# Kernel tuning notes

Hardware: AMD Instinct MI355X
Metric: run time of the kernel (lower is better)

Reference implementation:

```python
import jax, jax.numpy as jnp
import numpy as np

B, L, F, H, VOCAB = 32, 700, 4, 600, 2000  # batch, n_records(max_len), feats/record, hidden, vocab


def setup_inputs() -> dict:
    key = jax.random.key(0)
    ks = jax.random.split(key, 16)
    s = 0.02
    inp = {
        'records': jax.random.randint(ks[0], (B, L, F), 0, VOCAB, dtype=jnp.int64 if jax.config.jax_enable_x64 else jnp.int32),
        'index': jax.random.randint(ks[1], (B,), 0, L, dtype=jnp.int32),
        'emb': jax.random.normal(ks[2], (VOCAB, H), jnp.float32) * s,
        'W_relu': jax.random.normal(ks[3], (4 * H, H), jnp.float32) * s,
        'b_relu': jnp.zeros((H,), jnp.float32),
        'W_lin': jax.random.normal(ks[4], (H, H), jnp.float32) * s,
        'b_lin': jnp.zeros((H,), jnp.float32),
        'W_sig': jax.random.normal(ks[5], (2 * H, H), jnp.float32) * s,
        'b_sig': jnp.zeros((H,), jnp.float32),
        'W_ih': jax.random.normal(ks[6], (H, 4 * H), jnp.float32) * s,
        'W_hh': jax.random.normal(ks[7], (H, 4 * H), jnp.float32) * s,
        'b_ih': jnp.zeros((4 * H,), jnp.float32),
        'b_hh': jnp.zeros((4 * H,), jnp.float32),
        'W_log': jax.random.normal(ks[8], (H, L), jnp.float32) * s,
        'b_log': jnp.zeros((L,), jnp.float32),
    }
    return inp


def _select_content(records, emb, W_relu, b_relu, W_lin, b_lin, W_sig, b_sig):
    # embedding + concat of the 4 record features -> [B, L, 4H]
    embedded = emb[records]                               # [B, L, 4, H]
    emb_cat = embedded.reshape(records.shape[0], records.shape[1], -1)
    emb_relu = jax.nn.relu(emb_cat @ W_relu + b_relu)      # [B, L, H]
    emb_lin = emb_relu @ W_lin + b_lin                     # [B, L, H]
    pre_attn = jnp.einsum('bld,bmd->blm', emb_lin, emb_relu)  # [B, L, L]
    pad = (records.max(axis=2) == 0)                       # [B, L]
    mask = jnp.eye(records.shape[1], dtype=bool)[None] | pad[:, :, None] | pad[:, None, :]
    pre_attn = jnp.where(mask, -jnp.inf, pre_attn)
    attention = jax.nn.softmax(pre_attn, axis=2)
    emb_att = jnp.einsum('blm,bmd->bld', attention, emb_relu)  # [B, L, H]
    gate = jax.nn.sigmoid(jnp.concatenate([emb_relu, emb_att], axis=2) @ W_sig + b_sig)
    return gate * emb_relu                                 # selected_content [B, L, H]


def reference(records, index, emb, W_relu, b_relu, W_lin, b_lin, W_sig, b_sig,
              W_ih, W_hh, b_ih, b_hh, W_log, b_log):
    sc = _select_content(records, emb, W_relu, b_relu, W_lin, b_lin, W_sig, b_sig)
    # init_hidden
    hidden = jnp.mean(sc, axis=1)                          # [B, H]
    cell = jnp.zeros_like(hidden)
    pad_mask = (records.max(axis=2) == 0)                  # [B, L]
    # forward (one pointer step)
    b_idx = jnp.arange(records.shape[0])
    mask = pad_mask.at[b_idx, index].set(True)             # scatter_(1, index, 1)
    x = sc[b_idx, index]                                   # gather -> [B, H]
    gates = x @ W_ih + hidden @ W_hh + b_ih + b_hh         # [B, 4H]
    i, f, g, o = jnp.split(gates, 4, axis=1)               # torch LSTM gate order
    cell = jax.nn.sigmoid(f) * cell + jax.nn.sigmoid(i) * jnp.tanh(g)
    hidden = jax.nn.sigmoid(o) * jnp.tanh(cell)
    logits = hidden @ W_log + b_log                        # [B, max_len]
    masked = jnp.where(mask, -jnp.inf, logits)
    attention = jax.nn.log_softmax(masked, axis=1)         # [B, max_len]
    return attention, hidden, cell
```

## Files before the change

kernel.cpp:

```cpp
#include <hip/hip_runtime.h>
#include <math.h>

typedef unsigned short u16;
typedef _Float16 half8 __attribute__((ext_vector_type(8)));
typedef float f32x4 __attribute__((ext_vector_type(4)));

#define BB 32
#define LL 700
#define HH 600
#define VV 2000
#define H4 2400

#define O_SCAT   0L
#define O_LINH   57344000L
#define O_R1     86016000L
#define O_ATTNH  112896000L
#define O_ERT    144435200L
#define O_EMBH   171468800L
#define O_W2T    174028800L
#define O_WLT    177100800L
#define O_WST    177920000L
#define O_BL     179456000L
#define O_PAD    179458560L
#define O_GATES  179624960L
#define O_WIHT   179932160L
#define O_WLOGT  186076160L
#define O_XCAT   186977280L
#define O_HID16  187059200L
#define O_GLOG   187100160L

__device__ inline u16 f2h(float x) { _Float16 h = (_Float16)x; u16 u; __builtin_memcpy(&u, &h, 2); return u; }
__device__ inline float h2f(u16 u) { _Float16 h; __builtin_memcpy(&h, &u, 2); return (float)h; }
__device__ inline float to_f(float x) { return x; }
__device__ inline float to_f(u16 x) { return h2f(x); }

#define LROW 68
#define BUFSZ (128 * LROW)

template<int EPI>
__global__ __launch_bounds__(512, 4) void hgemm_k(
    const u16* __restrict__ A, const u16* __restrict__ B,
    float* __restrict__ C32, u16* __restrict__ C16,
    const float* __restrict__ bias, const u16* __restrict__ gate, int ldg,
    int M, int N, int Kp, int lda, int ldb, int ldc,
    long sA, long sB, long sC)
{
    const int bz = blockIdx.z;
    A += sA * bz;  B += sB * bz;
    if (EPI == 0) C32 += sC * bz; else C16 += sC * bz;

    __shared__ __align__(16) u16 As[2 * BUFSZ];
    __shared__ __align__(16) u16 Bs[2 * BUFSZ];

    const int tid  = threadIdx.x;

    const int nx = gridDim.x, ny = gridDim.y;
    const int bid = blockIdx.y * nx + blockIdx.x;
    const int fg  = ny >> 3;
    const int gsz = nx << 3;
    int m_i, n_i;
    if (bid < fg * gsz) {
        int g = bid / gsz, r = bid - g * gsz;
        m_i = (g << 3) + (r & 7);
        n_i = r >> 3;
    } else {
        m_i = bid / nx;
        n_i = bid - m_i * nx;
    }
    const int m0 = m_i << 7, n0 = n_i << 7;

    const int wave = tid >> 6, lane = tid & 63;
    const int wm = (wave >> 2) << 6;
    const int wn = (wave & 3) << 5;
    const int fr = lane & 15, q8 = (lane >> 4) << 3;

    const int lrow8 = lane >> 3;
    const int lcol8 = (lane & 7) << 3;
    int ar0 = m0 + (wave << 4) + lrow8;      if (ar0 > M - 1) ar0 = M - 1;
    int ar1 = m0 + (wave << 4) + 8 + lrow8;  if (ar1 > M - 1) ar1 = M - 1;
    int br0 = n0 + (wave << 4) + lrow8;      if (br0 > N - 1) br0 = N - 1;
    int br1 = n0 + (wave << 4) + 8 + lrow8;  if (br1 > N - 1) br1 = N - 1;
    const u16* gA0 = A + (long)ar0 * lda + lcol8;
    const u16* gA1 = A + (long)ar1 * lda + lcol8;
    const u16* gB0 = B + (long)br0 * ldb + lcol8;
    const u16* gB1 = B + (long)br1 * ldb + lcol8;
    const int lo0 = ((wave << 4) + lrow8) * LROW + lcol8;
    const int lo1 = lo0 + 8 * LROW;

    f32x4 acc[4][2];
    #pragma unroll
    for (int i = 0; i < 4; ++i)
        #pragma unroll
        for (int j = 0; j < 2; ++j) acc[i][j] = (f32x4)0.f;

    const int nk = Kp >> 6;
    uint4 pA0, pA1, pB0, pB1, qA0, qA1, qB0, qB1;

    pA0 = *(const uint4*)gA0;  pA1 = *(const uint4*)gA1;
    pB0 = *(const uint4*)gB0;  pB1 = *(const uint4*)gB1;
    *(uint4*)&As[lo0] = pA0;  *(uint4*)&As[lo1] = pA1;
    *(uint4*)&Bs[lo0] = pB0;  *(uint4*)&Bs[lo1] = pB1;
    if (nk > 1) {
        pA0 = *(const uint4*)(gA0 + 64);  pA1 = *(const uint4*)(gA1 + 64);
        pB0 = *(const uint4*)(gB0 + 64);  pB1 = *(const uint4*)(gB1 + 64);
    }
    __syncthreads();

    for (int s = 0; s < nk; ++s) {
        const int cur = (s & 1) * BUFSZ;
        if (s + 2 < nk) {
            const long ko = (long)(s + 2) << 6;
            qA0 = *(const uint4*)(gA0 + ko);  qA1 = *(const uint4*)(gA1 + ko);
            qB0 = *(const uint4*)(gB0 + ko);  qB1 = *(const uint4*)(gB1 + ko);
        }
        #pragma unroll
        for (int half = 0; half < 2; ++half) {
            const int kof = q8 + (half << 5);
            half8 af[4], bf[2];
            #pragma unroll
            for (int i = 0; i < 4; ++i) af[i] = *(const half8*)&As[cur + (wm + (i << 4) + fr) * LROW + kof];
            #pragma unroll
            for (int j = 0; j < 2; ++j) bf[j] = *(const half8*)&Bs[cur + (wn + (j << 4) + fr) * LROW + kof];
            #pragma unroll
            for (int i = 0; i < 4; ++i)
                #pragma unroll
                for (int j = 0; j < 2; ++j)
                    acc[i][j] = __builtin_amdgcn_mfma_f32_16x16x32_f16(af[i], bf[j], acc[i][j], 0, 0, 0);
        }
        if (s + 1 < nk) {
            const int nxt = ((s + 1) & 1) * BUFSZ;
            *(uint4*)&As[nxt + lo0] = pA0;  *(uint4*)&As[nxt + lo1] = pA1;
            *(uint4*)&Bs[nxt + lo0] = pB0;  *(uint4*)&Bs[nxt + lo1] = pB1;
        }
        pA0 = qA0;  pA1 = qA1;  pB0 = qB0;  pB1 = qB1;
        __syncthreads();
    }

    const int lr = (lane >> 4) << 2;
    #pragma unroll
    for (int j = 0; j < 2; ++j) {
        int n = n0 + wn + (j << 4) + fr;
        if (n >= N) continue;
        float bv = bias ? bias[n] : 0.f;
        #pragma unroll
        for (int i = 0; i < 4; ++i) {
            #pragma unroll
            for (int r = 0; r < 4; ++r) {
                int m = m0 + wm + (i << 4) + lr + r;
                if (m >= M) continue;
                long off = (long)m * ldc + n;
                float v = acc[i][j][r] + bv;
                if (EPI == 0) C32[off] = v;
                if (EPI == 1) C16[off] = f2h(v);
                if (EPI == 2) {
                    float sg = 1.f / (1.f + expf(-v));
                    C16[off] = f2h(sg * h2f(gate[(long)m * ldg + n]));
                }
            }
        }
    }
}

__global__ __launch_bounds__(256) void sgemm_k(
    const u16* __restrict__ A, const u16* __restrict__ B, float* __restrict__ C,
    int N, int Kseg, int lda, int ldb, int ldc)
{
    const int wave = threadIdx.x >> 6, lane = threadIdx.x & 63;
    const int fr = lane & 15, q8 = (lane >> 4) << 3;
    int n = blockIdx.x * 64 + wave * 16 + fr;
    int nc = (n < N) ? n : N - 1;
    const int k0 = blockIdx.y * Kseg;
    const u16* pa0 = A + (long)fr * lda + q8;
    const u16* pa1 = A + (long)(fr + 16) * lda + q8;
    const u16* pb  = B + (long)nc * ldb + q8;
    f32x4 acc0 = (f32x4)0.f, acc1 = (f32x4)0.f;
    #pragma unroll 2
    for (int k = k0; k < k0 + Kseg; k += 32) {
        half8 a0 = *(const half8*)(pa0 + k);
        half8 a1 = *(const half8*)(pa1 + k);
        half8 bv = *(const half8*)(pb + k);
        acc0 = __builtin_amdgcn_mfma_f32_16x16x32_f16(a0, bv, acc0, 0, 0, 0);
        acc1 = __builtin_amdgcn_mfma_f32_16x16x32_f16(a1, bv, acc1, 0, 0, 0);
    }
    if (n >= N) return;
    const int mr = (lane >> 4) << 2;
    #pragma unroll
    for (int r = 0; r < 4; ++r) {
        atomicAdd(&C[(long)(mr + r) * ldc + n], acc0[r]);
        atomicAdd(&C[(long)(mr + r + 16) * ldc + n], acc1[r]);
    }
}

__global__ __launch_bounds__(256) void prep_k(
    const float* __restrict__ emb, const float* __restrict__ W_relu,
    const float* __restrict__ W_lin, const float* __restrict__ W_sig,
    const float* __restrict__ W_ih, const float* __restrict__ W_hh,
    const float* __restrict__ W_log, const float* __restrict__ b_lin,
    const float* __restrict__ b_ih, const float* __restrict__ b_hh,
    const float* __restrict__ b_log,
    u16* __restrict__ embh, u16* __restrict__ w2t, u16* __restrict__ wlt,
    u16* __restrict__ wst, u16* __restrict__ wiht, u16* __restrict__ wlogt,
    float* __restrict__ bl640, float* __restrict__ gates, float* __restrict__ glog)
{
    __shared__ float t[32][33];
    const int z = blockIdx.z, bx = blockIdx.x, by = blockIdx.y;
    const int tid = threadIdx.x;

    if (z == 10) {
        int r = by * 32 + (tid >> 5), c = bx * 32 + (tid & 31);
        #pragma unroll
        for (int dy = 0; dy < 32; dy += 8) {
            int rr = r + dy;
            if (rr < VV && c < 640)
                embh[(long)rr * 640 + c] = (c < 600) ? f2h(emb[(long)rr * 600 + c]) : 0;
        }
        return;
    }
    if (z == 11) {
        long idx = ((long)bx * 75 + by) * 256 + tid;
        if (idx < 640) {
            bl640[idx] = (idx < 600) ? b_lin[idx] : 0.f;
        } else if (idx < 640 + (long)BB * H4) {
            long i = idx - 640;
            int n = (int)(i % H4);
            gates[i] = b_ih[n] + b_hh[n];
        } else if (idx < 640 + (long)BB * H4 + (long)BB * 704) {
            long i = idx - 640 - (long)BB * H4;
            int l = (int)(i % 704);
            glog[i] = (l < 700) ? b_log[l] : 0.f;
        }
        return;
    }

    const float* s; u16* d;
    int R, C, lds_, ldo, Rpad, Cpad;
    if (z < 4)      { s = W_relu + 360000L * z; d = w2t + 384000L * z;
                      R = 600; C = 600; lds_ = 600; ldo = 640;  Rpad = 640; Cpad = 600; }
    else if (z == 4){ s = W_lin;           d = wlt;
                      R = 600; C = 600; lds_ = 600; ldo = 640;  Rpad = 640; Cpad = 640; }
    else if (z == 5){ s = W_sig;           d = wst;
                      R = 600; C = 600; lds_ = 600; ldo = 1280; Rpad = 640; Cpad = 600; }
    else if (z == 6){ s = W_sig + 360000;  d = wst + 640;
                      R = 600; C = 600; lds_ = 600; ldo = 1280; Rpad = 640; Cpad = 600; }
    else if (z == 7){ s = W_ih;            d = wiht;
                      R = 600; C = H4;  lds_ = H4;  ldo = 1280; Rpad = 640; Cpad = H4; }
    else if (z == 8){ s = W_hh;            d = wiht + 640;
                      R = 600; C = H4;  lds_ = H4;  ldo = 1280; Rpad = 640; Cpad = H4; }
    else            { s = W_log;           d = wlogt;
                      R = 600; C = 700; lds_ = 700; ldo = 640;  Rpad = 640; Cpad = 704; }

    int r0 = bx * 32, c0 = by * 32;
    if (r0 >= Rpad || c0 >= Cpad) return;
    int tx = tid & 31, ty = tid >> 5;
    #pragma unroll
    for (int dy = 0; dy < 32; dy += 8) {
        int r = r0 + ty + dy, c = c0 + tx;
        t[ty + dy][tx] = (r < R && c < C) ? s[(long)r * lds_ + c] : 0.f;
    }
    __syncthreads();
    #pragma unroll
    for (int dy = 0; dy < 32; dy += 8) {
        int c = c0 + ty + dy, r = r0 + tx;
        if (r < Rpad && c < Cpad) d[(long)c * ldo + r] = f2h(t[tx][ty + dy]);
    }
}

template<typename T>
__global__ __launch_bounds__(256) void transpz_k(
    const T* __restrict__ s, u16* __restrict__ d,
    int R, int C, int lds_, int ldo, int Rpad, int Cpad, long zs_s, long zs_d)
{
    __shared__ float t[32][33];
    s += zs_s * blockIdx.z;  d += zs_d * blockIdx.z;
    int r0 = blockIdx.x * 32, c0 = blockIdx.y * 32;
    int tx = threadIdx.x & 31, ty = threadIdx.x >> 5;
    #pragma unroll
    for (int dy = 0; dy < 32; dy += 8) {
        int r = r0 + ty + dy, c = c0 + tx;
        t[ty + dy][tx] = (r < R && c < C) ? to_f(s[(long)r * lds_ + c]) : 0.f;
    }
    __syncthreads();
    #pragma unroll
    for (int dy = 0; dy < 32; dy += 8) {
        int c = c0 + ty + dy, r = r0 + tx;
        if (r < Rpad && c < Cpad) d[(long)c * ldo + r] = f2h(t[tx][ty + dy]);
    }
}

__global__ __launch_bounds__(320) void gather_relu_k(
    const int* __restrict__ rec, const u16* __restrict__ Ph,
    const float* __restrict__ b_relu, u16* __restrict__ scat, float* __restrict__ pad)
{
    int row = blockIdx.x;
    int t = threadIdx.x;
    int r0 = rec[row * 4 + 0], r1 = rec[row * 4 + 1];
    int r2 = rec[row * 4 + 2], r3 = rec[row * 4 + 3];
    u16* srow = scat + (long)row * 1280;
    if (t < 300) {
        int h = t << 1;
        uint a0 = *(const uint*)&Ph[(long)r0 * H4 + h];
        uint a1 = *(const uint*)&Ph[(long)r1 * H4 + 600 + h];
        uint a2 = *(const uint*)&Ph[(long)r2 * H4 + 1200 + h];
        uint a3 = *(const uint*)&Ph[(long)r3 * H4 + 1800 + h];
        float lo = b_relu[h]     + h2f((u16)a0) + h2f((u16)a1) + h2f((u16)a2) + h2f((u16)a3);
        float hi = b_relu[h + 1] + h2f((u16)(a0 >> 16)) + h2f((u16)(a1 >> 16))
                                 + h2f((u16)(a2 >> 16)) + h2f((u16)(a3 >> 16));
        uint o = (uint)f2h(fmaxf(lo, 0.f)) | ((uint)f2h(fmaxf(hi, 0.f)) << 16);
        *(uint*)&srow[h] = o;
    } else {
        int i = t - 300;
        *(uint*)&srow[600 + (i << 1)]  = 0;
        *(uint*)&srow[1240 + (i << 1)] = 0;
    }
    if (t == 0) {
        int mx = max(max(r0, r1), max(r2, r3));
        pad[row] = (mx == 0) ? 1.f : 0.f;
    }
}

__global__ __launch_bounds__(256) void softmax_w(u16* __restrict__ attnh,
                                                 const float* __restrict__ pad)
{
    const int wave = threadIdx.x >> 6, lane = threadIdx.x & 63;
    const int l = blockIdx.x * 4 + wave, b = blockIdx.y;
    u16* row = attnh + (long)b * (LL * 704) + (long)l * 704;
    const float* pb = pad + b * LL;
    const bool rowpad = pb[l] != 0.f;

    float v[12];
    float mx = -INFINITY;
    #pragma unroll
    for (int i = 0; i < 6; ++i) {
        int e0 = (lane + (i << 6)) << 1;
        float x0 = -INFINITY, x1 = -INFINITY;
        if (e0 < 704) {
            uint u = *(const uint*)&row[e0];
            if (e0 < LL && !(rowpad || e0 == l || pb[e0] != 0.f)) x0 = h2f((u16)u);
            int e1 = e0 + 1;
            if (e1 < LL && !(rowpad || e1 == l || pb[e1] != 0.f)) x1 = h2f((u16)(u >> 16));
        }
        v[2 * i] = x0;  v[2 * i + 1] = x1;
        mx = fmaxf(mx, fmaxf(x0, x1));
    }
    #pragma unroll
    for (int m = 32; m > 0; m >>= 1) mx = fmaxf(mx, __shfl_xor(mx, m));
    mx = fmaxf(mx, -1e30f);

    float sum = 0.f;
    #pragma unroll
    for (int i = 0; i < 12; ++i) { v[i] = expf(v[i] - mx); sum += v[i]; }
    #pragma unroll
    for (int m = 32; m > 0; m >>= 1) sum += __shfl_xor(sum, m);
    float inv = (sum > 0.f) ? 1.f / sum : 0.f;

    #pragma unroll
    for (int i = 0; i < 6; ++i) {
        int e0 = (lane + (i << 6)) << 1;
        if (e0 < 704) {
            uint u = (uint)f2h(v[2 * i] * inv) | ((uint)f2h(v[2 * i + 1] * inv) << 16);
            *(uint*)&row[e0] = u;
        }
    }
}

__global__ __launch_bounds__(256) void xcat_k(const u16* __restrict__ sc,
                                              const int* __restrict__ index,
                                              u16* __restrict__ xcat)
{
    int b = blockIdx.y;
    if (blockIdx.x == 3) {
        const u16* src = sc + ((long)b * LL + index[b]) * HH;
        u16* dst = xcat + b * 1280;
        for (int j = threadIdx.x; j < 1280; j += 256) {
            if (j < 600) dst[j] = src[j];
            else if (j < 640) dst[j] = 0;
            else if (j >= 1240) dst[j] = 0;
        }
        return;
    }
    int h = blockIdx.x * 256 + threadIdx.x;
    if (h >= HH) return;
    float s = 0.f;
    const u16* base = sc + (long)b * LL * HH + h;
    for (int l = 0; l < LL; ++l) s += h2f(base[(long)l * HH]);
    xcat[b * 1280 + 640 + h] = f2h(s * (1.f / 700.f));
}

__global__ void lstm_act_k(const float* __restrict__ gates,
                           float* __restrict__ out_hid, float* __restrict__ out_cell,
                           u16* __restrict__ hid16)
{
    int h = blockIdx.x * 256 + threadIdx.x;
    int b = blockIdx.y;
    if (h >= 640) return;
    if (h >= HH) { hid16[b * 640 + h] = 0; return; }
    const float* g = gates + b * H4;
    float gi = g[h], gg = g[1200 + h], go = g[1800 + h];
    float c = (1.f / (1.f + expf(-gi))) * tanhf(gg);
    float hd = (1.f / (1.f + expf(-go))) * tanhf(c);
    out_hid[b * HH + h] = hd;
    out_cell[b * HH + h] = c;
    hid16[b * 640 + h] = f2h(hd);
}

__global__ __launch_bounds__(256) void logsoftmax_k(const float* __restrict__ glog,
                                                    const float* __restrict__ pad,
                                                    const int* __restrict__ index,
                                                    float* __restrict__ out)
{
    int b = blockIdx.x;
    int t = threadIdx.x;
    int idx = index[b];
    __shared__ float red[256];
    float v[3];
    float mx = -INFINITY;
    #pragma unroll
    for (int ii = 0; ii < 3; ++ii) {
        int l = ii * 256 + t;
        float x = -INFINITY;
        if (l < LL && !(pad[b * LL + l] != 0.f || l == idx)) x = glog[b * 704 + l];
        v[ii] = x;
        mx = fmaxf(mx, x);
    }
    red[t] = mx; __syncthreads();
    for (int s = 128; s > 0; s >>= 1) {
        if (t < s) red[t] = fmaxf(red[t], red[t + s]);
        __syncthreads();
    }
    mx = red[0]; __syncthreads();
    float sum = 0.f;
    #pragma unroll
    for (int ii = 0; ii < 3; ++ii) {
        int l = ii * 256 + t;
        if (l < LL) sum += expf(v[ii] - mx);
    }
    red[t] = sum; __syncthreads();
    for (int s = 128; s > 0; s >>= 1) {
        if (t < s) red[t] += red[t + s];
        __syncthreads();
    }
    float lse = mx + logf(red[0]);
    #pragma unroll
    for (int ii = 0; ii < 3; ++ii) {
        int l = ii * 256 + t;
        if (l < LL) out[b * LL + l] = fmaxf(v[ii] - lse, -1e30f);
    }
}

extern "C" void kernel_launch(void* const* d_in, const int* in_sizes, int n_in,
                              void* d_out, int out_size, void* d_ws, size_t ws_size,
                              hipStream_t stream)
{
    const int*   records = (const int*)d_in[0];
    const int*   index   = (const int*)d_in[1];
    const float* emb     = (const float*)d_in[2];
    const float* W_relu  = (const float*)d_in[3];
    const float* b_relu  = (const float*)d_in[4];
    const float* W_lin   = (const float*)d_in[5];
    const float* b_lin   = (const float*)d_in[6];
    const float* W_sig   = (const float*)d_in[7];
    const float* b_sig   = (const float*)d_in[8];
    const float* W_ih    = (const float*)d_in[9];
    const float* W_hh    = (const float*)d_in[10];
    const float* b_ih    = (const float*)d_in[11];
    const float* b_hh    = (const float*)d_in[12];
    const float* W_log   = (const float*)d_in[13];
    const float* b_log   = (const float*)d_in[14];

    char* ws = (char*)d_ws;
    u16*   scat   = (u16*)(ws + O_SCAT);
    u16*   linh   = (u16*)(ws + O_LINH);
    u16*   Ph     = (u16*)(ws + O_R1);
    u16*   sc16   = (u16*)(ws + O_R1);
    u16*   attnh  = (u16*)(ws + O_ATTNH);
    u16*   erT    = (u16*)(ws + O_ERT);
    u16*   embh   = (u16*)(ws + O_EMBH);
    u16*   w2t    = (u16*)(ws + O_W2T);
    u16*   wlt    = (u16*)(ws + O_WLT);
    u16*   wst    = (u16*)(ws + O_WST);
    float* bl640  = (float*)(ws + O_BL);
    float* pad    = (float*)(ws + O_PAD);
    float* gates  = (float*)(ws + O_GATES);
    u16*   wiht   = (u16*)(ws + O_WIHT);
    u16*   wlogt  = (u16*)(ws + O_WLOGT);
    u16*   xcat   = (u16*)(ws + O_XCAT);
    u16*   hid16  = (u16*)(ws + O_HID16);
    float* glog   = (float*)(ws + O_GLOG);

    float* out      = (float*)d_out;
    float* out_attn = out;
    float* out_hid  = out + BB * LL;
    float* out_cell = out + BB * LL + BB * HH;

    prep_k<<<dim3(20, 75, 12), 256, 0, stream>>>(
        emb, W_relu, W_lin, W_sig, W_ih, W_hh, W_log, b_lin, b_ih, b_hh, b_log,
        embh, w2t, wlt, wst, wiht, wlogt, bl640, gates, glog);

    hgemm_k<1><<<dim3(19, 16, 1), 512, 0, stream>>>(
        embh, w2t, nullptr, Ph, nullptr, nullptr, 0,
        VV, H4, 640, 640, 640, H4, 0L, 0L, 0L);

    gather_relu_k<<<dim3(BB * LL), 320, 0, stream>>>(records, Ph, b_relu, scat, pad);

    hgemm_k<1><<<dim3(5, 175, 1), 512, 0, stream>>>(
        scat, wlt, nullptr, linh, bl640, nullptr, 0,
        BB * LL, 640, 640, 1280, 640, 640, 0L, 0L, 0L);

    hgemm_k<1><<<dim3(6, 6, BB), 512, 0, stream>>>(
        linh, scat, nullptr, attnh, nullptr, nullptr, 0,
        LL, LL, 640, 640, 1280, 704, (long)LL * 640, (long)LL * 1280, (long)LL * 704);

    softmax_w<<<dim3(175, BB), 256, 0, stream>>>(attnh, pad);

    transpz_k<u16><<<dim3(22, 19, BB), 256, 0, stream>>>(
        scat, erT, 700, 600, 1280, 704, 704, 600, (long)700 * 1280, (long)600 * 704);

    hgemm_k<1><<<dim3(5, 6, BB), 512, 0, stream>>>(
        attnh, erT, nullptr, scat + 640, nullptr, nullptr, 0,
        LL, HH, 704, 704, 704, 1280, (long)LL * 704, (long)HH * 704, (long)LL * 1280);

    hgemm_k<2><<<dim3(5, 175, 1), 512, 0, stream>>>(
        scat, wst, nullptr, sc16, b_sig, scat, 1280,
        BB * LL, HH, 1280, 1280, 1280, HH, 0L, 0L, 0L);

    xcat_k<<<dim3(4, BB), 256, 0, stream>>>(sc16, index, xcat);
    sgemm_k<<<dim3(38, 5), 256, 0, stream>>>(
        xcat, wiht, gates, H4, 256, 1280, 1280, H4);
    lstm_act_k<<<dim3(3, BB), 256, 0, stream>>>(gates, out_hid, out_cell, hid16);
    sgemm_k<<<dim3(11, 5), 256, 0, stream>>>(
        hid16, wlogt, glog, LL, 128, 640, 640, 704);
    logsoftmax_k<<<dim3(BB), 256, 0, stream>>>(glog, pad, index, out_attn);
}
```

Measured before the change: 454.4 us.

## Add 256x256-tile HGEMM with direct global-to-LDS loads for the main GEMMs

Adds a new fp16 MFMA GEMM kernel with 256x256 output tiles and 8 waves, each wave computing 128x64. It loads A and B straight into LDS with global_load_lds and interleaves those loads with the MFMA phases under explicit waitcnt and barrier control. Tiles are visited in grouped order for L2 reuse, and the work runs at raised wave priority. It replaces the older 128-tile kernel for the linear, attention-score, attention-apply and sigmoid-gate GEMMs, aiming for more data reuse per tile and better overlap of loads with compute. In exchange, the larger tiles waste more work on ragged edges (700 and 600 are not multiples of 256), give smaller grids, and depend on hand-written synchronisation being correct.

```diff
diff --git a/kernel.cpp b/kernel.cpp
--- a/kernel.cpp
+++ b/kernel.cpp
@@ -33,6 +33,149 @@
 __device__ inline float h2f(u16 u) { _Float16 h; __builtin_memcpy(&h, &u, 2); return (float)h; }
 __device__ inline float to_f(float x) { return x; }
 __device__ inline float to_f(u16 x) { return h2f(x); }
+
+__device__ __forceinline__ void gll16(const u16* g, u16* l) {
+    __builtin_amdgcn_global_load_lds(
+        (__attribute__((address_space(1))) void*)g,
+        (__attribute__((address_space(3))) void*)l, 16, 0, 0);
+}
+
+#define BARX  asm volatile("s_barrier" ::: "memory")
+#define LGKM0 asm volatile("s_waitcnt lgkmcnt(0)" ::: "memory")
+#define VM6   asm volatile("s_waitcnt vmcnt(6)" ::: "memory")
+#define VM0   asm volatile("s_waitcnt vmcnt(0)" ::: "memory")
+#define SB0   __builtin_amdgcn_sched_barrier(0)
+
+#define RD_B(base) { _Pragma("unroll") for (int j = 0; j < 4; ++j) \
+    bfr[j] = *(const half8*)&Bs[(base) + ((wn64 + (j << 4) + fr) << 5) + swr]; }
+#define RD_A(base, IOFF) { _Pragma("unroll") for (int i = 0; i < 4; ++i) \
+    afr[i] = *(const half8*)&As[(base) + ((wm128 + ((i + IOFF) << 4) + fr) << 5) + swr]; }
+#define MFMA16(IOFF) \
+    LGKM0; SB0; \
+    __builtin_amdgcn_s_setprio(1); \
+    _Pragma("unroll") for (int i = 0; i < 4; ++i) \
+        _Pragma("unroll") for (int j = 0; j < 4; ++j) \
+            acc[i + IOFF][j] = __builtin_amdgcn_mfma_f32_16x16x32_f16(afr[i], bfr[j], acc[i + IOFF][j], 0, 0, 0); \
+    __builtin_amdgcn_s_setprio(0); SB0;
+
+template<int EPI>
+__global__ __launch_bounds__(512, 2) void hgemm256_k(
+    const u16* __restrict__ A, const u16* __restrict__ B,
+    u16* __restrict__ C16, const float* __restrict__ bias,
+    const u16* __restrict__ gate, int ldg,
+    int M, int N, int Kp, int lda, int ldb, int ldc,
+    long sAz, long sBz, long sCz)
+{
+    const int bz = blockIdx.z;
+    A += sAz * bz;  B += sBz * bz;  C16 += sCz * bz;
+
+    __shared__ __align__(16) u16 As[32768];
+    __shared__ __align__(16) u16 Bs[32768];
+
+    const int tid = threadIdx.x;
+
+    const int nx = gridDim.x, ny = gridDim.y;
+    const int bid = blockIdx.y * nx + blockIdx.x;
+    const int fg  = ny >> 3;
+    const int gsz = nx << 3;
+    int m_i, n_i;
+    if (bid < fg * gsz) {
+        int g = bid / gsz, r = bid - g * gsz;
+        m_i = (g << 3) + (r & 7);
+        n_i = r >> 3;
+    } else {
+        m_i = bid / nx;
+        n_i = bid - m_i * nx;
+    }
+    const int m0 = m_i << 8, n0 = n_i << 8;
+
+    const int wave = tid >> 6, lane = tid & 63;
+    const int fr = lane & 15;
+    const int swr = (((lane >> 4) ^ ((lane >> 1) & 3)) << 3);
+    const int wm128 = (wave >> 2) << 7;
+    const int wn64  = (wave & 3) << 6;
+
+    const int srow = (wave << 5) + (lane >> 2);
+    const int kx   = (((lane & 3) ^ ((lane >> 3) & 3)) << 3);
+    int ra0 = m0 + srow;        if (ra0 > M - 1) ra0 = M - 1;
+    int ra1 = m0 + srow + 16;   if (ra1 > M - 1) ra1 = M - 1;
+    int rb0 = n0 + srow;        if (rb0 > N - 1) rb0 = N - 1;
+    int rb1 = n0 + srow + 16;   if (rb1 > N - 1) rb1 = N - 1;
+    const u16* gA0 = A + (long)ra0 * lda + kx;
+    const u16* gA1 = A + (long)ra1 * lda + kx;
+    const u16* gB0 = B + (long)rb0 * ldb + kx;
+    const u16* gB1 = B + (long)rb1 * ldb + kx;
+    u16* sA = (u16*)As + (wave << 10);
+    u16* sB = (u16*)Bs + (wave << 10);
+
+    f32x4 acc[8][4];
+    #pragma unroll
+    for (int i = 0; i < 8; ++i)
+        #pragma unroll
+        for (int j = 0; j < 4; ++j) acc[i][j] = (f32x4)0.f;
+
+    const int nk = Kp >> 6;
+
+    gll16(gA0, sA);             gll16(gA1, sA + 512);
+    gll16(gB0, sB);             gll16(gB1, sB + 512);
+    gll16(gA0 + 32, sA + 8192); gll16(gA1 + 32, sA + 8192 + 512);
+    gll16(gB0 + 32, sB + 8192); gll16(gB1 + 32, sB + 8192 + 512);
+
+    for (int t = 0; t < nk; ++t) {
+        const int bo  = (t & 1) << 14;
+        const int nbo = bo ^ 16384;
+        const long ko = (long)((t + 1 < nk) ? t + 1 : t) << 6;
+        half8 afr[4], bfr[4];
+
+        gll16(gA0 + ko, sA + nbo);  gll16(gA1 + ko, sA + nbo + 512);
+        VM6; BARX;
+        RD_B(bo); RD_A(bo, 0);
+        MFMA16(0);
+        BARX;
+
+        gll16(gB0 + ko, sB + nbo);  gll16(gB1 + ko, sB + nbo + 512);
+        RD_A(bo, 4);
+        BARX;
+        MFMA16(4);
+        BARX;
+
+        gll16(gA0 + ko + 32, sA + nbo + 8192);  gll16(gA1 + ko + 32, sA + nbo + 8192 + 512);
+        VM6; BARX;
+        RD_B(bo + 8192); RD_A(bo + 8192, 0);
+        MFMA16(0);
+        BARX;
+
+        gll16(gB0 + ko + 32, sB + nbo + 8192);  gll16(gB1 + ko + 32, sB + nbo + 8192 + 512);
+        RD_A(bo + 8192, 4);
+        BARX;
+        MFMA16(4);
+        BARX;
+    }
+    VM0;
+
+    const int lr = (lane >> 4) << 2;
+    #pragma unroll
+    for (int j = 0; j < 4; ++j) {
+        int n = n0 + wn64 + (j << 4) + fr;
+        if (n >= N) continue;
+        float bv = bias ? bias[n] : 0.f;
+        #pragma unroll
+        for (int i = 0; i < 8; ++i) {
+            #pragma unroll
+            for (int r = 0; r < 4; ++r) {
+                int m = m0 + wm128 + (i << 4) + lr + r;
+                if (m >= M) continue;
+                long off = (long)m * ldc + n;
+                float v = acc[i][j][r] + bv;
+                if (EPI == 1) C16[off] = f2h(v);
+                if (EPI == 2) {
+                    float sg = 1.f / (1.f + expf(-v));
+                    C16[off] = f2h(sg * h2f(gate[(long)m * ldg + n]));
+                }
+            }
+        }
+    }
+}
 
 #define LROW 68
 #define BUFSZ (128 * LROW)
@@ -502,12 +645,12 @@
 
     gather_relu_k<<<dim3(BB * LL), 320, 0, stream>>>(records, Ph, b_relu, scat, pad);
 
-    hgemm_k<1><<<dim3(5, 175, 1), 512, 0, stream>>>(
-        scat, wlt, nullptr, linh, bl640, nullptr, 0,
+    hgemm256_k<1><<<dim3(3, 88, 1), 512, 0, stream>>>(
+        scat, wlt, linh, bl640, nullptr, 0,
         BB * LL, 640, 640, 1280, 640, 640, 0L, 0L, 0L);
 
-    hgemm_k<1><<<dim3(6, 6, BB), 512, 0, stream>>>(
-        linh, scat, nullptr, attnh, nullptr, nullptr, 0,
+    hgemm256_k<1><<<dim3(3, 3, BB), 512, 0, stream>>>(
+        linh, scat, attnh, nullptr, nullptr, 0,
         LL, LL, 640, 640, 1280, 704, (long)LL * 640, (long)LL * 1280, (long)LL * 704);
 
     softmax_w<<<dim3(175, BB), 256, 0, stream>>>(attnh, pad);
@@ -515,13 +658,13 @@
     transpz_k<u16><<<dim3(22, 19, BB), 256, 0, stream>>>(
         scat, erT, 700, 600, 1280, 704, 704, 600, (long)700 * 1280, (long)600 * 704);
 
-    hgemm_k<1><<<dim3(5, 6, BB), 512, 0, stream>>>(
-        attnh, erT, nullptr, scat + 640, nullptr, nullptr, 0,
+    hgemm256_k<1><<<dim3(3, 3, BB), 512, 0, stream>>>(
+        attnh, erT, scat + 640, nullptr, nullptr, 0,
         LL, HH, 704, 704, 704, 1280, (long)LL * 704, (long)HH * 704, (long)LL * 1280);
 
-    hgemm_k<2><<<dim3(5, 175, 1), 512, 0, stream>>>(
-        scat, wst, nullptr, sc16, b_sig, scat, 1280,
-        BB * LL, HH, 1280, 1280, 1280, HH, 0L, 0L, 0L);
+    hgemm256_k<2><<<dim3(3, 88, 1), 512, 0, stream>>>(
+        scat, wst, sc16, b_sig, scat, 1280,
+        BB * LL, HH, 1280, 1280, 1280, 600, 0L, 0L, 0L);
 
     xcat_k<<<dim3(4, BB), 256, 0, stream>>>(sc16, index, xcat);
     sgemm_k<<<dim3(38, 5), 256, 0, stream>>>(
```

New measurement: 617.7 us. +35.9%, slower.

## Add direct-to-LDS double-buffered MFMA GEMM with swizzled LDS and grouped tile order

Applied to the files above, without the earlier changes.

Introduces a new fp16 GEMM kernel that stages A and B tiles straight from global memory into LDS with global_load_lds. It double-buffers 64-wide K slices in an XOR-swizzled LDS layout and remaps block indices into groups of eight M tiles for L2 reuse. All five half-precision GEMM launches switch to it, with the same bias and sigmoid-gate epilogues. This aims to skip the register round trip on tile loads and cut LDS bank conflicts, but it uses a single barrier per K step and clamps out-of-range rows instead of zero-filling them.

```diff
diff --git a/kernel.cpp b/kernel.cpp
--- a/kernel.cpp
+++ b/kernel.cpp
@@ -33,6 +33,125 @@
 __device__ inline float h2f(u16 u) { _Float16 h; __builtin_memcpy(&h, &u, 2); return (float)h; }
 __device__ inline float to_f(float x) { return x; }
 __device__ inline float to_f(u16 x) { return h2f(x); }
+
+__device__ __forceinline__ void gll16(const u16* g, u16* l) {
+    __builtin_amdgcn_global_load_lds(
+        (__attribute__((address_space(1))) void*)g,
+        (__attribute__((address_space(3))) void*)l, 16, 0, 0);
+}
+
+template<int EPI>
+__global__ __launch_bounds__(512, 4) void hgemm_v2(
+    const u16* __restrict__ A, const u16* __restrict__ B,
+    u16* __restrict__ C16, const float* __restrict__ bias,
+    const u16* __restrict__ gate, int ldg,
+    int M, int N, int Kp, int lda, int ldb, int ldc,
+    long sAz, long sBz, long sCz)
+{
+    const int bz = blockIdx.z;
+    A += sAz * bz;  B += sBz * bz;  C16 += sCz * bz;
+
+    __shared__ __align__(16) u16 As[16384];
+    __shared__ __align__(16) u16 Bs[16384];
+
+    const int tid = threadIdx.x;
+
+    const int nx = gridDim.x, ny = gridDim.y;
+    const int bid = blockIdx.y * nx + blockIdx.x;
+    const int fg  = ny >> 3;
+    const int gsz = nx << 3;
+    int m_i, n_i;
+    if (bid < fg * gsz) {
+        int g = bid / gsz, r = bid - g * gsz;
+        m_i = (g << 3) + (r & 7);
+        n_i = r >> 3;
+    } else {
+        m_i = bid / nx;
+        n_i = bid - m_i * nx;
+    }
+    const int m0 = m_i << 7, n0 = n_i << 7;
+
+    const int wave = tid >> 6, lane = tid & 63;
+    const int fr = lane & 15, q = lane >> 4;
+    const int s0 = (q ^ (fr & 7)) << 3;
+    const int wm = (wave >> 2) << 6;
+    const int wn = (wave & 3) << 5;
+
+    const int srow = lane >> 3;
+    const int kx   = ((lane & 7) ^ srow) << 3;
+    int ra0 = m0 + (wave << 4) + srow;       if (ra0 > M - 1) ra0 = M - 1;
+    int ra1 = m0 + (wave << 4) + 8 + srow;   if (ra1 > M - 1) ra1 = M - 1;
+    int rb0 = n0 + (wave << 4) + srow;       if (rb0 > N - 1) rb0 = N - 1;
+    int rb1 = n0 + (wave << 4) + 8 + srow;   if (rb1 > N - 1) rb1 = N - 1;
+    const u16* gA0 = A + (long)ra0 * lda + kx;
+    const u16* gA1 = A + (long)ra1 * lda + kx;
+    const u16* gB0 = B + (long)rb0 * ldb + kx;
+    const u16* gB1 = B + (long)rb1 * ldb + kx;
+    u16* sAw = (u16*)As + (wave << 10);
+    u16* sBw = (u16*)Bs + (wave << 10);
+
+    f32x4 acc[4][2];
+    #pragma unroll
+    for (int i = 0; i < 4; ++i)
+        #pragma unroll
+        for (int j = 0; j < 2; ++j) acc[i][j] = (f32x4)0.f;
+
+    const int nk = Kp >> 6;
+
+    gll16(gA0, sAw);  gll16(gA1, sAw + 512);
+    gll16(gB0, sBw);  gll16(gB1, sBw + 512);
+    __syncthreads();
+
+    for (int t = 0; t < nk; ++t) {
+        const int cur = (t & 1) << 13;
+        if (t + 1 < nk) {
+            const int nxt = cur ^ 8192;
+            const long ko = (long)(t + 1) << 6;
+            gll16(gA0 + ko, sAw + nxt);  gll16(gA1 + ko, sAw + nxt + 512);
+            gll16(gB0 + ko, sBw + nxt);  gll16(gB1 + ko, sBw + nxt + 512);
+        }
+        #pragma unroll
+        for (int half = 0; half < 2; ++half) {
+            const int sh = s0 ^ (half << 5);
+            half8 af[4], bf[2];
+            #pragma unroll
+            for (int i = 0; i < 4; ++i)
+                af[i] = *(const half8*)&As[cur + ((wm + (i << 4) + fr) << 6) + sh];
+            #pragma unroll
+            for (int j = 0; j < 2; ++j)
+                bf[j] = *(const half8*)&Bs[cur + ((wn + (j << 4) + fr) << 6) + sh];
+            #pragma unroll
+            for (int i = 0; i < 4; ++i)
+                #pragma unroll
+                for (int j = 0; j < 2; ++j)
+                    acc[i][j] = __builtin_amdgcn_mfma_f32_16x16x32_f16(af[i], bf[j], acc[i][j], 0, 0, 0);
+        }
+        __syncthreads();
+    }
+
+    const int lr = (lane >> 4) << 2;
+    #pragma unroll
+    for (int j = 0; j < 2; ++j) {
+        int n = n0 + wn + (j << 4) + fr;
+        if (n >= N) continue;
+        float bv = bias ? bias[n] : 0.f;
+        #pragma unroll
+        for (int i = 0; i < 4; ++i) {
+            #pragma unroll
+            for (int r = 0; r < 4; ++r) {
+                int m = m0 + wm + (i << 4) + lr + r;
+                if (m >= M) continue;
+                long off = (long)m * ldc + n;
+                float v = acc[i][j][r] + bv;
+                if (EPI == 1) C16[off] = f2h(v);
+                if (EPI == 2) {
+                    float sg = 1.f / (1.f + expf(-v));
+                    C16[off] = f2h(sg * h2f(gate[(long)m * ldg + n]));
+                }
+            }
+        }
+    }
+}
 
 #define LROW 68
 #define BUFSZ (128 * LROW)
@@ -496,18 +615,18 @@
         emb, W_relu, W_lin, W_sig, W_ih, W_hh, W_log, b_lin, b_ih, b_hh, b_log,
         embh, w2t, wlt, wst, wiht, wlogt, bl640, gates, glog);
 
-    hgemm_k<1><<<dim3(19, 16, 1), 512, 0, stream>>>(
-        embh, w2t, nullptr, Ph, nullptr, nullptr, 0,
+    hgemm_v2<1><<<dim3(19, 16, 1), 512, 0, stream>>>(
+        embh, w2t, Ph, nullptr, nullptr, 0,
         VV, H4, 640, 640, 640, H4, 0L, 0L, 0L);
 
     gather_relu_k<<<dim3(BB * LL), 320, 0, stream>>>(records, Ph, b_relu, scat, pad);
 
-    hgemm_k<1><<<dim3(5, 175, 1), 512, 0, stream>>>(
-        scat, wlt, nullptr, linh, bl640, nullptr, 0,
+    hgemm_v2<1><<<dim3(5, 175, 1), 512, 0, stream>>>(
+        scat, wlt, linh, bl640, nullptr, 0,
         BB * LL, 640, 640, 1280, 640, 640, 0L, 0L, 0L);
 
-    hgemm_k<1><<<dim3(6, 6, BB), 512, 0, stream>>>(
-        linh, scat, nullptr, attnh, nullptr, nullptr, 0,
+    hgemm_v2<1><<<dim3(6, 6, BB), 512, 0, stream>>>(
+        linh, scat, attnh, nullptr, nullptr, 0,
         LL, LL, 640, 640, 1280, 704, (long)LL * 640, (long)LL * 1280, (long)LL * 704);
 
     softmax_w<<<dim3(175, BB), 256, 0, stream>>>(attnh, pad);
@@ -515,13 +634,13 @@
     transpz_k<u16><<<dim3(22, 19, BB), 256, 0, stream>>>(
         scat, erT, 700, 600, 1280, 704, 704, 600, (long)700 * 1280, (long)600 * 704);
 
-    hgemm_k<1><<<dim3(5, 6, BB), 512, 0, stream>>>(
-        attnh, erT, nullptr, scat + 640, nullptr, nullptr, 0,
+    hgemm_v2<1><<<dim3(5, 6, BB), 512, 0, stream>>>(
+        attnh, erT, scat + 640, nullptr, nullptr, 0,
         LL, HH, 704, 704, 704, 1280, (long)LL * 704, (long)HH * 704, (long)LL * 1280);
 
-    hgemm_k<2><<<dim3(5, 175, 1), 512, 0, stream>>>(
-        scat, wst, nullptr, sc16, b_sig, scat, 1280,
-        BB * LL, HH, 1280, 1280, 1280, HH, 0L, 0L, 0L);
+    hgemm_v2<2><<<dim3(5, 175, 1), 512, 0, stream>>>(
+        scat, wst, sc16, b_sig, scat, 1280,
+        BB * LL, HH, 1280, 1280, 1280, 600, 0L, 0L, 0L);
 
     xcat_k<<<dim3(4, BB), 256, 0, stream>>>(sc16, index, xcat);
     sgemm_k<<<dim3(38, 5), 256, 0, stream>>>(
```

Result: faster. 435.8 us (-4.1%).

## Load GEMM tiles directly into LDS with swizzled layout and smaller K-step

Applied to the files above, without the earlier changes.

Rewrites the half-precision GEMM main loop to use global_load_lds so tiles go straight from global memory into shared memory without passing through registers. The K-step shrinks from 64 to 32 and the padded rows are replaced by an XOR-swizzled 32-wide layout. This cuts LDS use and register pressure enough to raise the occupancy hint from 4 to 8 blocks. In exchange the loop runs twice as many iterations, each with a barrier, and each prefetch is only one stage deep.

```diff
diff --git a/kernel.cpp b/kernel.cpp
--- a/kernel.cpp
+++ b/kernel.cpp
@@ -34,25 +34,27 @@
 __device__ inline float to_f(float x) { return x; }
 __device__ inline float to_f(u16 x) { return h2f(x); }
 
-#define LROW 68
-#define BUFSZ (128 * LROW)
+__device__ __forceinline__ void gll16(const u16* g, u16* l) {
+    __builtin_amdgcn_global_load_lds(
+        (__attribute__((address_space(1))) void*)g,
+        (__attribute__((address_space(3))) void*)l, 16, 0, 0);
+}
 
 template<int EPI>
-__global__ __launch_bounds__(512, 4) void hgemm_k(
+__global__ __launch_bounds__(512, 8) void hgemm_v3(
     const u16* __restrict__ A, const u16* __restrict__ B,
-    float* __restrict__ C32, u16* __restrict__ C16,
-    const float* __restrict__ bias, const u16* __restrict__ gate, int ldg,
+    u16* __restrict__ C16, const float* __restrict__ bias,
+    const u16* __restrict__ gate, int ldg,
     int M, int N, int Kp, int lda, int ldb, int ldc,
-    long sA, long sB, long sC)
+    long sAz, long sBz, long sCz)
 {
     const int bz = blockIdx.z;
-    A += sA * bz;  B += sB * bz;
-    if (EPI == 0) C32 += sC * bz; else C16 += sC * bz;
-
-    __shared__ __align__(16) u16 As[2 * BUFSZ];
-    __shared__ __align__(16) u16 Bs[2 * BUFSZ];
-
-    const int tid  = threadIdx.x;
+    A += sAz * bz;  B += sBz * bz;  C16 += sCz * bz;
+
+    __shared__ __align__(16) u16 As[8192];
+    __shared__ __align__(16) u16 Bs[8192];
+
+    const int tid = threadIdx.x;
 
     const int nx = gridDim.x, ny = gridDim.y;
     const int bid = blockIdx.y * nx + blockIdx.x;
@@ -70,22 +72,19 @@
     const int m0 = m_i << 7, n0 = n_i << 7;
 
     const int wave = tid >> 6, lane = tid & 63;
+    const int fr = lane & 15, q = lane >> 4;
+    const int srd = (q ^ ((fr >> 1) & 3)) << 3;
     const int wm = (wave >> 2) << 6;
     const int wn = (wave & 3) << 5;
-    const int fr = lane & 15, q8 = (lane >> 4) << 3;
-
-    const int lrow8 = lane >> 3;
-    const int lcol8 = (lane & 7) << 3;
-    int ar0 = m0 + (wave << 4) + lrow8;      if (ar0 > M - 1) ar0 = M - 1;
-    int ar1 = m0 + (wave << 4) + 8 + lrow8;  if (ar1 > M - 1) ar1 = M - 1;
-    int br0 = n0 + (wave << 4) + lrow8;      if (br0 > N - 1) br0 = N - 1;
-    int br1 = n0 + (wave << 4) + 8 + lrow8;  if (br1 > N - 1) br1 = N - 1;
-    const u16* gA0 = A + (long)ar0 * lda + lcol8;
-    const u16* gA1 = A + (long)ar1 * lda + lcol8;
-    const u16* gB0 = B + (long)br0 * ldb + lcol8;
-    const u16* gB1 = B + (long)br1 * ldb + lcol8;
-    const int lo0 = ((wave << 4) + lrow8) * LROW + lcol8;
-    const int lo1 = lo0 + 8 * LROW;
+
+    const int srow = lane >> 2;
+    const int kx   = ((lane & 3) ^ ((srow >> 1) & 3)) << 3;
+    int ra = m0 + (wave << 4) + srow;   if (ra > M - 1) ra = M - 1;
+    int rb = n0 + (wave << 4) + srow;   if (rb > N - 1) rb = N - 1;
+    const u16* gA = A + (long)ra * lda + kx;
+    const u16* gB = B + (long)rb * ldb + kx;
+    u16* sAw = (u16*)As + (wave << 9);
+    u16* sBw = (u16*)Bs + (wave << 9);
 
     f32x4 acc[4][2];
     #pragma unroll
@@ -93,46 +92,30 @@
         #pragma unroll
         for (int j = 0; j < 2; ++j) acc[i][j] = (f32x4)0.f;
 
-    const int nk = Kp >> 6;
-    uint4 pA0, pA1, pB0, pB1, qA0, qA1, qB0, qB1;
-
-    pA0 = *(const uint4*)gA0;  pA1 = *(const uint4*)gA1;
-    pB0 = *(const uint4*)gB0;  pB1 = *(const uint4*)gB1;
-    *(uint4*)&As[lo0] = pA0;  *(uint4*)&As[lo1] = pA1;
-    *(uint4*)&Bs[lo0] = pB0;  *(uint4*)&Bs[lo1] = pB1;
-    if (nk > 1) {
-        pA0 = *(const uint4*)(gA0 + 64);  pA1 = *(const uint4*)(gA1 + 64);
-        pB0 = *(const uint4*)(gB0 + 64);  pB1 = *(const uint4*)(gB1 + 64);
-    }
+    const int nk = Kp >> 5;
+
+    gll16(gA, sAw);  gll16(gB, sBw);
     __syncthreads();
 
-    for (int s = 0; s < nk; ++s) {
-        const int cur = (s & 1) * BUFSZ;
-        if (s + 2 < nk) {
-            const long ko = (long)(s + 2) << 6;
-            qA0 = *(const uint4*)(gA0 + ko);  qA1 = *(const uint4*)(gA1 + ko);
-            qB0 = *(const uint4*)(gB0 + ko);  qB1 = *(const uint4*)(gB1 + ko);
-        }
+    for (int t = 0; t < nk; ++t) {
+        const int cur = (t & 1) << 12;
+        if (t + 1 < nk) {
+            const int nxt = cur ^ 4096;
+            const long ko = (long)(t + 1) << 5;
+            gll16(gA + ko, sAw + nxt);  gll16(gB + ko, sBw + nxt);
+        }
+        half8 af[4], bf[2];
         #pragma unroll
-        for (int half = 0; half < 2; ++half) {
-            const int kof = q8 + (half << 5);
-            half8 af[4], bf[2];
+        for (int i = 0; i < 4; ++i)
+            af[i] = *(const half8*)&As[cur + ((wm + (i << 4) + fr) << 5) + srd];
+        #pragma unroll
+        for (int j = 0; j < 2; ++j)
+            bf[j] = *(const half8*)&Bs[cur + ((wn + (j << 4) + fr) << 5) + srd];
+        #pragma unroll
+        for (int i = 0; i < 4; ++i)
             #pragma unroll
-            for (int i = 0; i < 4; ++i) af[i] = *(const half8*)&As[cur + (wm + (i << 4) + fr) * LROW + kof];
-            #pragma unroll
-            for (int j = 0; j < 2; ++j) bf[j] = *(const half8*)&Bs[cur + (wn + (j << 4) + fr) * LROW + kof];
-            #pragma unroll
-            for (int i = 0; i < 4; ++i)
-                #pragma unroll
-                for (int j = 0; j < 2; ++j)
-                    acc[i][j] = __builtin_amdgcn_mfma_f32_16x16x32_f16(af[i], bf[j], acc[i][j], 0, 0, 0);
-        }
-        if (s + 1 < nk) {
-            const int nxt = ((s + 1) & 1) * BUFSZ;
-            *(uint4*)&As[nxt + lo0] = pA0;  *(uint4*)&As[nxt + lo1] = pA1;
-            *(uint4*)&Bs[nxt + lo0] = pB0;  *(uint4*)&Bs[nxt + lo1] = pB1;
-        }
-        pA0 = qA0;  pA1 = qA1;  pB0 = qB0;  pB1 = qB1;
+            for (int j = 0; j < 2; ++j)
+                acc[i][j] = __builtin_amdgcn_mfma_f32_16x16x32_f16(af[i], bf[j], acc[i][j], 0, 0, 0);
         __syncthreads();
     }
 
@@ -150,7 +133,6 @@
                 if (m >= M) continue;
                 long off = (long)m * ldc + n;
                 float v = acc[i][j][r] + bv;
-                if (EPI == 0) C32[off] = v;
                 if (EPI == 1) C16[off] = f2h(v);
                 if (EPI == 2) {
                     float sg = 1.f / (1.f + expf(-v));
@@ -496,18 +478,18 @@
         emb, W_relu, W_lin, W_sig, W_ih, W_hh, W_log, b_lin, b_ih, b_hh, b_log,
         embh, w2t, wlt, wst, wiht, wlogt, bl640, gates, glog);
 
-    hgemm_k<1><<<dim3(19, 16, 1), 512, 0, stream>>>(
-        embh, w2t, nullptr, Ph, nullptr, nullptr, 0,
+    hgemm_v3<1><<<dim3(19, 16, 1), 512, 0, stream>>>(
+        embh, w2t, Ph, nullptr, nullptr, 0,
         VV, H4, 640, 640, 640, H4, 0L, 0L, 0L);
 
     gather_relu_k<<<dim3(BB * LL), 320, 0, stream>>>(records, Ph, b_relu, scat, pad);
 
-    hgemm_k<1><<<dim3(5, 175, 1), 512, 0, stream>>>(
-        scat, wlt, nullptr, linh, bl640, nullptr, 0,
+    hgemm_v3<1><<<dim3(5, 175, 1), 512, 0, stream>>>(
+        scat, wlt, linh, bl640, nullptr, 0,
         BB * LL, 640, 640, 1280, 640, 640, 0L, 0L, 0L);
 
-    hgemm_k<1><<<dim3(6, 6, BB), 512, 0, stream>>>(
-        linh, scat, nullptr, attnh, nullptr, nullptr, 0,
+    hgemm_v3<1><<<dim3(6, 6, BB), 512, 0, stream>>>(
+        linh, scat, attnh, nullptr, nullptr, 0,
         LL, LL, 640, 640, 1280, 704, (long)LL * 640, (long)LL * 1280, (long)LL * 704);
 
     softmax_w<<<dim3(175, BB), 256, 0, stream>>>(attnh, pad);
@@ -515,13 +497,13 @@
     transpz_k<u16><<<dim3(22, 19, BB), 256, 0, stream>>>(
         scat, erT, 700, 600, 1280, 704, 704, 600, (long)700 * 1280, (long)600 * 704);
 
-    hgemm_k<1><<<dim3(5, 6, BB), 512, 0, stream>>>(
-        attnh, erT, nullptr, scat + 640, nullptr, nullptr, 0,
+    hgemm_v3<1><<<dim3(5, 6, BB), 512, 0, stream>>>(
+        attnh, erT, scat + 640, nullptr, nullptr, 0,
         LL, HH, 704, 704, 704, 1280, (long)LL * 704, (long)HH * 704, (long)LL * 1280);
 
-    hgemm_k<2><<<dim3(5, 175, 1), 512, 0, stream>>>(
-        scat, wst, nullptr, sc16, b_sig, scat, 1280,
-        BB * LL, HH, 1280, 1280, 1280, HH, 0L, 0L, 0L);
+    hgemm_v3<2><<<dim3(5, 175, 1), 512, 0, stream>>>(
+        scat, wst, sc16, b_sig, scat, 1280,
+        BB * LL, HH, 1280, 1280, 1280, 600, 0L, 0L, 0L);
 
     xcat_k<<<dim3(4, BB), 256, 0, stream>>>(sc16, index, xcat);
     sgemm_k<<<dim3(38, 5), 256, 0, stream>>>(
```

Measured after the change: 463.4 us. No clear change (+2.0%).
